# Performance work log

Hardware: AMD Instinct MI355X
Metric: run time of the kernel (lower is better)

Reference implementation:

```python
import jax, jax.numpy as jnp
import numpy as np

LATENT = 8
HIDDEN = 16
DFEAT = 16
N_LAYERS = 10
G = 64          # num graphs
NPG = 1024      # nodes per graph
E = G * NPG * 16  # edges (avg degree 16)


def setup_inputs() -> dict:
    key = jax.random.key(0)
    ks = jax.random.split(key, 20)
    n = G * NPG
    x = jax.random.normal(ks[0], (n, DFEAT), dtype=jnp.float32)
    eps = jax.random.normal(ks[1], (n, LATENT), dtype=jnp.float32)
    # edges constrained to lie within a graph (block-diagonal structure)
    g = jax.random.randint(ks[2], (E,), 0, G)
    ls = jax.random.randint(ks[3], (E,), 0, NPG)
    ld = jax.random.randint(ks[4], (E,), 0, NPG)
    edge_index = jnp.stack([g * NPG + ls, g * NPG + ld]).astype(jnp.int32)
    s = 0.1
    inp = {
        "x": x, "eps": eps, "edge_index": edge_index, "num_graphs": G,
        # GIN layer 0 MLP (lazy in_channels -> hidden -> hidden)
        "W0a": jax.random.normal(ks[5], (DFEAT, HIDDEN), jnp.float32) * s,
        "b0a": jnp.zeros((HIDDEN,), jnp.float32),
        "W0b": jax.random.normal(ks[6], (HIDDEN, HIDDEN), jnp.float32) * s,
        "b0b": jnp.zeros((HIDDEN,), jnp.float32),
        # GIN layers 1..9 MLPs, stacked
        "Wa": jax.random.normal(ks[7], (N_LAYERS - 1, HIDDEN, HIDDEN), jnp.float32) * s,
        "ba": jnp.zeros((N_LAYERS - 1, HIDDEN), jnp.float32),
        "Wb": jax.random.normal(ks[8], (N_LAYERS - 1, HIDDEN, HIDDEN), jnp.float32) * s,
        "bb": jnp.zeros((N_LAYERS - 1, HIDDEN), jnp.float32),
        # mean / std heads
        "Wm": jax.random.normal(ks[9], (HIDDEN, LATENT), jnp.float32) * s,
        "bm": jnp.zeros((LATENT,), jnp.float32),
        "Ws": jax.random.normal(ks[10], (HIDDEN, LATENT), jnp.float32) * s,
        "bs": jnp.zeros((LATENT,), jnp.float32),
    }
    return inp


def _gin_encode(x, edge_index, W0a, b0a, W0b, b0b, Wa, ba, Wb, bb):
    n = x.shape[0]
    src, dst = edge_index[0], edge_index[1]

    def conv(h, wa, bia, wb, bib):
        # GINConv, eps=0: MLP((1+eps)*h + sum_{j in N(i)} h_j)
        agg = h + jax.ops.segment_sum(h[src], dst, num_segments=n)
        return jax.nn.relu(agg @ wa + bia) @ wb + bib

    h = jax.nn.relu(conv(x, W0a, b0a, W0b, b0b))
    for i in range(Wa.shape[0]):
        h = conv(h, Wa[i], ba[i], Wb[i], bb[i])
        if i < Wa.shape[0] - 1:  # act between layers, not after the last conv
            h = jax.nn.relu(h)
    return h


def _vae_forward(x, eps, edge_index, num_graphs,
                 W0a, b0a, W0b, b0b, Wa, ba, Wb, bb, Wm, bm, Ws, bs):
    n = x.shape[0]
    npg = n // num_graphs
    h = _gin_encode(x, edge_index, W0a, b0a, W0b, b0b, Wa, ba, Wb, bb)
    mu = h @ Wm + bm
    std = jax.nn.softplus(h @ Ws + bs)
    z = mu + std * eps                      # rsample from Normal(mu, std)
    z3 = z.reshape(num_graphs, npg, LATENT)  # per-graph split (equal sizes)
    # inner-product decode per graph, sigmoid act
    adj_pred = jax.nn.sigmoid(jnp.einsum("gnd,gmd->gnm", z3, z3))
    # to_dense_adj on the block-diagonal edge list
    src, dst = edge_index[0], edge_index[1]
    g = src // npg
    dense_adj = jnp.zeros((num_graphs, npg, npg), jnp.float32)
    dense_adj = dense_adj.at[g, src % npg, dst % npg].set(1.0)
    # BCELoss(reduction='sum') with torch's log clamp at -100
    logp = jnp.clip(jnp.log(adj_pred), -100.0)
    log1mp = jnp.clip(jnp.log1p(-adj_pred), -100.0)
    nll = -jnp.sum(dense_adj * logp + (1.0 - dense_adj) * log1mp)
    # KL(N(mu,std) || N(0,1)), summed
    kl = jnp.sum(-jnp.log(std) + 0.5 * (std * std + mu * mu) - 0.5)
    return nll, kl, adj_pred, dense_adj


def reference(x, eps, edge_index, num_graphs,
              W0a, b0a, W0b, b0b, Wa, ba, Wb, bb, Wm, bm, Ws, bs):
    return _vae_forward(x, eps, edge_index, num_graphs,
                        W0a, b0a, W0b, b0b, Wa, ba, Wb, bb, Wm, bm, Ws, bs)
```

## Files before the change

kernel.cpp:

```cpp
#include <hip/hip_runtime.h>
#include <cstddef>

#define G 64
#define NPG 1024
#define NNODES 65536
#define NEDGE 1048576
#define BCAP 48
#define LCAP 32
#define HSTR 20
#define ZTR 1028
#define ADJ_ELEMS 67108864ull
#define BM_WORDS 2097152

typedef float f32x4 __attribute__((ext_vector_type(4)));
typedef float f32x2 __attribute__((ext_vector_type(2)));
typedef unsigned u32x4 __attribute__((ext_vector_type(4)));

__global__ __launch_bounds__(1024) void k_init(int* __restrict__ cnt, float* __restrict__ acc,
                                               unsigned* __restrict__ bm) {
  int i = blockIdx.x * 1024 + threadIdx.x;
  cnt[i] = 0;
  if (i < 2) acc[i] = 0.0f;
  u32x4 z = {0u, 0u, 0u, 0u};
  u32x4* b4 = (u32x4*)bm;
  for (int k = i; k < BM_WORDS / 4; k += 65536) b4[k] = z;
}

__global__ __launch_bounds__(256) void k_build(const int* __restrict__ ei,
                                               int* __restrict__ cnt,
                                               unsigned short* __restrict__ colb,
                                               unsigned* __restrict__ bm) {
  int t = blockIdx.x * 256 + threadIdx.x;
  const int4* sp = (const int4*)ei;
  const int4* dp = (const int4*)(ei + NEDGE);
  int4 s4 = sp[t];
  int4 d4 = dp[t];
  int ss[4] = {s4.x, s4.y, s4.z, s4.w};
  int dd[4] = {d4.x, d4.y, d4.z, d4.w};
  #pragma unroll
  for (int q = 0; q < 4; ++q) {
    int src = ss[q], dst = dd[q];
    int p = atomicAdd(&cnt[dst], 1);
    if (p < BCAP) colb[(size_t)dst * BCAP + p] = (unsigned short)(src & (NPG - 1));
    int gg = src >> 10, ls = src & (NPG - 1), ld = dst & (NPG - 1);
    atomicOr(&bm[gg * 32768 + ls * 32 + (ld >> 5)], 1u << (ld & 31));
  }
}

__global__ __launch_bounds__(1024) void k_gin(
    const float* __restrict__ x, const float* __restrict__ eps,
    const int* __restrict__ cnt, const unsigned short* __restrict__ colb,
    const float* __restrict__ W0a, const float* __restrict__ b0a,
    const float* __restrict__ W0b, const float* __restrict__ b0b,
    const float* __restrict__ Wa, const float* __restrict__ ba,
    const float* __restrict__ Wb, const float* __restrict__ bb,
    const float* __restrict__ Wm, const float* __restrict__ bm_,
    const float* __restrict__ Ws, const float* __restrict__ bs,
    const unsigned* __restrict__ ebm,
    float* __restrict__ zbuf, float* __restrict__ acc, float* __restrict__ out) {
  __shared__ float hbuf[NPG * HSTR];
  __shared__ unsigned short colc[NPG * LCAP];
  __shared__ float red[16];

  if (blockIdx.x >= G) {
    f32x4* dz = (f32x4*)(out + 2 + ADJ_ELEMS);
    size_t i = (size_t)(blockIdx.x - G) * 1024 + threadIdx.x;
    size_t stride = (size_t)(gridDim.x - G) * 1024;
    for (; i < ADJ_ELEMS / 4; i += stride) {
      unsigned w = ebm[i >> 3];
      int sh = ((int)i & 7) << 2;
      f32x4 v;
      v.x = ((w >> (sh + 0)) & 1) ? 1.f : 0.f;
      v.y = ((w >> (sh + 1)) & 1) ? 1.f : 0.f;
      v.z = ((w >> (sh + 2)) & 1) ? 1.f : 0.f;
      v.w = ((w >> (sh + 3)) & 1) ? 1.f : 0.f;
      __builtin_nontemporal_store(v, &dz[i]);
    }
    return;
  }

  const int g = blockIdx.x;
  const int tid = threadIdx.x;
  const int dv0 = cnt[g * NPG + tid];
  const int dv = (dv0 < BCAP) ? dv0 : BCAP;
  const int dvl = (dv < LCAP) ? dv : LCAP;
  const unsigned short* cl = colb + (size_t)(g * NPG + tid) * BCAP;

  {
    const uint4* rowp = (const uint4*)(colb + (size_t)(g * NPG + tid) * BCAP);
    #pragma unroll
    for (int q = 0; q < 2; ++q) {
    }
    #pragma unroll
    for (int q = 0; q < 4; ++q) {
      uint4 w4 = rowp[q];
      unsigned ws0 = w4.x, ws1 = w4.y, ws2 = w4.z, ws3 = w4.w;
      colc[(q * 8 + 0) * NPG + tid] = (unsigned short)(ws0 & 0xffff);
      colc[(q * 8 + 1) * NPG + tid] = (unsigned short)(ws0 >> 16);
      colc[(q * 8 + 2) * NPG + tid] = (unsigned short)(ws1 & 0xffff);
      colc[(q * 8 + 3) * NPG + tid] = (unsigned short)(ws1 >> 16);
      colc[(q * 8 + 4) * NPG + tid] = (unsigned short)(ws2 & 0xffff);
      colc[(q * 8 + 5) * NPG + tid] = (unsigned short)(ws2 >> 16);
      colc[(q * 8 + 6) * NPG + tid] = (unsigned short)(ws3 & 0xffff);
      colc[(q * 8 + 7) * NPG + tid] = (unsigned short)(ws3 >> 16);
    }
  }

  {
    const float4* xg = (const float4*)(x + (size_t)g * (NPG * 16));
    for (int idx = tid; idx < NPG * 4; idx += 1024) {
      float4 v = xg[idx];
      *(float4*)(hbuf + (idx >> 2) * HSTR + (idx & 3) * 4) = v;
    }
  }
  __syncthreads();

  for (int l = 0; l < 10; ++l) {
    const float* Aw = (l == 0) ? W0a : Wa + (l - 1) * 256;
    const float* Ab = (l == 0) ? b0a : ba + (l - 1) * 16;
    const float* Bw = (l == 0) ? W0b : Wb + (l - 1) * 256;
    const float* Bb = (l == 0) ? b0b : bb + (l - 1) * 16;

    float4 a0 = *(const float4*)(hbuf + tid * HSTR + 0);
    float4 a1 = *(const float4*)(hbuf + tid * HSTR + 4);
    float4 a2 = *(const float4*)(hbuf + tid * HSTR + 8);
    float4 a3 = *(const float4*)(hbuf + tid * HSTR + 12);
    for (int k = 0; k < dvl; ++k) {
      int ls = colc[k * NPG + tid];
      const float* hp = hbuf + ls * HSTR;
      float4 v0 = *(const float4*)(hp + 0);
      float4 v1 = *(const float4*)(hp + 4);
      float4 v2 = *(const float4*)(hp + 8);
      float4 v3 = *(const float4*)(hp + 12);
      a0.x += v0.x; a0.y += v0.y; a0.z += v0.z; a0.w += v0.w;
      a1.x += v1.x; a1.y += v1.y; a1.z += v1.z; a1.w += v1.w;
      a2.x += v2.x; a2.y += v2.y; a2.z += v2.z; a2.w += v2.w;
      a3.x += v3.x; a3.y += v3.y; a3.z += v3.z; a3.w += v3.w;
    }
    for (int k = LCAP; k < dv; ++k) {
      int ls = cl[k];
      const float* hp = hbuf + ls * HSTR;
      float4 v0 = *(const float4*)(hp + 0);
      float4 v1 = *(const float4*)(hp + 4);
      float4 v2 = *(const float4*)(hp + 8);
      float4 v3 = *(const float4*)(hp + 12);
      a0.x += v0.x; a0.y += v0.y; a0.z += v0.z; a0.w += v0.w;
      a1.x += v1.x; a1.y += v1.y; a1.z += v1.z; a1.w += v1.w;
      a2.x += v2.x; a2.y += v2.y; a2.z += v2.z; a2.w += v2.w;
      a3.x += v3.x; a3.y += v3.y; a3.z += v3.z; a3.w += v3.w;
    }
    float aa[16] = {a0.x, a0.y, a0.z, a0.w, a1.x, a1.y, a1.z, a1.w,
                    a2.x, a2.y, a2.z, a2.w, a3.x, a3.y, a3.z, a3.w};

    float u[16], v[16];
    #pragma unroll
    for (int j = 0; j < 16; ++j) u[j] = Ab[j];
    #pragma unroll
    for (int i = 0; i < 16; ++i) {
      float ai = aa[i];
      #pragma unroll
      for (int j = 0; j < 16; ++j) u[j] += ai * Aw[i * 16 + j];
    }
    #pragma unroll
    for (int j = 0; j < 16; ++j) u[j] = fmaxf(u[j], 0.f);
    #pragma unroll
    for (int j = 0; j < 16; ++j) v[j] = Bb[j];
    #pragma unroll
    for (int i = 0; i < 16; ++i) {
      float ui = u[i];
      #pragma unroll
      for (int j = 0; j < 16; ++j) v[j] += ui * Bw[i * 16 + j];
    }
    const bool rl = (l != 9);
    __syncthreads();
    #pragma unroll
    for (int j4 = 0; j4 < 4; ++j4) {
      float4 w;
      w.x = rl ? fmaxf(v[j4 * 4 + 0], 0.f) : v[j4 * 4 + 0];
      w.y = rl ? fmaxf(v[j4 * 4 + 1], 0.f) : v[j4 * 4 + 1];
      w.z = rl ? fmaxf(v[j4 * 4 + 2], 0.f) : v[j4 * 4 + 2];
      w.w = rl ? fmaxf(v[j4 * 4 + 3], 0.f) : v[j4 * 4 + 3];
      *(float4*)(hbuf + tid * HSTR + j4 * 4) = w;
    }
    __syncthreads();
  }

  float hv[16];
  #pragma unroll
  for (int i = 0; i < 16; ++i) hv[i] = hbuf[tid * HSTR + i];

  float mu[8], st[8];
  #pragma unroll
  for (int m = 0; m < 8; ++m) { mu[m] = bm_[m]; st[m] = bs[m]; }
  #pragma unroll
  for (int i = 0; i < 16; ++i) {
    float hi = hv[i];
    #pragma unroll
    for (int m = 0; m < 8; ++m) { mu[m] += hi * Wm[i * 8 + m]; st[m] += hi * Ws[i * 8 + m]; }
  }
  #pragma unroll
  for (int m = 0; m < 8; ++m) {
    float s = st[m];
    st[m] = fmaxf(s, 0.f) + log1pf(__expf(-fabsf(s)));
  }
  int gid = g * NPG + tid;
  float4 e0 = *(const float4*)(eps + (size_t)gid * 8);
  float4 e1 = *(const float4*)(eps + (size_t)gid * 8 + 4);
  float ev[8] = {e0.x, e0.y, e0.z, e0.w, e1.x, e1.y, e1.z, e1.w};
  float zv[8];
  float klp = 0.f;
  #pragma unroll
  for (int m = 0; m < 8; ++m) {
    zv[m] = mu[m] + st[m] * ev[m];
    klp += -__logf(st[m]) + 0.5f * (st[m] * st[m] + mu[m] * mu[m]) - 0.5f;
  }
  *(float4*)(zbuf + (size_t)gid * 8) = make_float4(zv[0], zv[1], zv[2], zv[3]);
  *(float4*)(zbuf + (size_t)gid * 8 + 4) = make_float4(zv[4], zv[5], zv[6], zv[7]);

  for (int o = 32; o > 0; o >>= 1) klp += __shfl_down(klp, o, 64);
  if ((tid & 63) == 0) red[tid >> 6] = klp;
  __syncthreads();
  if (tid == 0) {
    float s = 0.f;
    for (int i = 0; i < 16; ++i) s += red[i];
    atomicAdd(&acc[1], s);
  }
}

__device__ __forceinline__ float elem_p(float sv, int bit, float& accl) {
  float t = __expf(-sv);
  float p = __builtin_amdgcn_rcpf(1.f + t);
  float lp, lm;
  if (t > 3.0e38f)             { lp = -100.f; lm = 0.f; }
  else if (t < 5.9604645e-08f) { lp = 0.f;    lm = -100.f; }
  else { float q = __logf(1.f + t); lp = -q; lm = -sv - q; }
  accl += bit ? lp : lm;
  return p;
}

__global__ __launch_bounds__(256) void k_adj(const float* __restrict__ zbuf,
                                             const unsigned* __restrict__ ebm,
                                             float* __restrict__ out,
                                             float* __restrict__ acc) {
  __shared__ float zt[8 * ZTR];
  __shared__ float red[4];
  const int tid = threadIdx.x;
  const int g = blockIdx.x >> 6;
  const int i0 = (blockIdx.x & 63) << 4;

  {
    const float4* zg = (const float4*)(zbuf + (size_t)g * (NPG * 8));
    #pragma unroll
    for (int it = 0; it < 8; ++it) {
      int idx = tid + it * 256;
      float4 v = zg[idx];
      int j = idx >> 1, db = (idx & 1) << 2;
      zt[(db + 0) * ZTR + j] = v.x;
      zt[(db + 1) * ZTR + j] = v.y;
      zt[(db + 2) * ZTR + j] = v.z;
      zt[(db + 3) * ZTR + j] = v.w;
    }
  }
  __syncthreads();

  const int w = tid >> 6;
  const int l = tid & 63;
  float accl = 0.f;

  for (int ir = 0; ir < 4; ++ir) {
    const int i = i0 + (w << 2) + ir;
    float zi[8];
    #pragma unroll
    for (int d = 0; d < 8; ++d) zi[d] = zt[d * ZTR + i];
    const unsigned* bmrow = ebm + g * 32768 + i * 32;
    float* orow = out + 2 + (size_t)g * (NPG * NPG) + (size_t)i * NPG;
    #pragma unroll
    for (int jp = 0; jp < 4; ++jp) {
      const int j0 = (l << 2) + (jp << 8);
      float s0 = 0.f, s1 = 0.f, s2 = 0.f, s3 = 0.f;
      #pragma unroll
      for (int d = 0; d < 8; ++d) {
        float4 zr = *(const float4*)(zt + d * ZTR + j0);
        float zd = zi[d];
        s0 += zd * zr.x; s1 += zd * zr.y; s2 += zd * zr.z; s3 += zd * zr.w;
      }
      unsigned bits = (bmrow[j0 >> 5] >> (j0 & 31)) & 15u;
      float p0 = elem_p(s0, bits & 1, accl);
      float p1 = elem_p(s1, (bits >> 1) & 1, accl);
      float p2 = elem_p(s2, (bits >> 2) & 1, accl);
      float p3 = elem_p(s3, (bits >> 3) & 1, accl);
      f32x2 v0 = {p0, p1}, v1 = {p2, p3};
      f32x2* dp = (f32x2*)(orow + j0);
      __builtin_nontemporal_store(v0, &dp[0]);
      __builtin_nontemporal_store(v1, &dp[1]);
    }
  }

  for (int o = 32; o > 0; o >>= 1) accl += __shfl_down(accl, o, 64);
  if (l == 0) red[w] = accl;
  __syncthreads();
  if (tid == 0) atomicAdd(&acc[0], red[0] + red[1] + red[2] + red[3]);
}

__global__ void k_fin(const float* __restrict__ acc, float* __restrict__ out) {
  if (threadIdx.x == 0 && blockIdx.x == 0) {
    out[0] = -acc[0];
    out[1] = acc[1];
  }
}

extern "C" void kernel_launch(void* const* d_in, const int* in_sizes, int n_in,
                              void* d_out, int out_size, void* d_ws, size_t ws_size,
                              hipStream_t stream) {
  const float* x   = (const float*)d_in[0];
  const float* eps = (const float*)d_in[1];
  const int*   ei  = (const int*)d_in[2];
  const float* W0a = (const float*)d_in[4];
  const float* b0a = (const float*)d_in[5];
  const float* W0b = (const float*)d_in[6];
  const float* b0b = (const float*)d_in[7];
  const float* Wa  = (const float*)d_in[8];
  const float* ba  = (const float*)d_in[9];
  const float* Wb  = (const float*)d_in[10];
  const float* bb  = (const float*)d_in[11];
  const float* Wm  = (const float*)d_in[12];
  const float* bm  = (const float*)d_in[13];
  const float* Ws  = (const float*)d_in[14];
  const float* bs  = (const float*)d_in[15];
  float* out = (float*)d_out;

  int* cnt             = (int*)d_ws;
  unsigned short* colb = (unsigned short*)(cnt + NNODES);
  float* zbuf          = (float*)(colb + (size_t)NNODES * BCAP);
  unsigned* ebm        = (unsigned*)(zbuf + (size_t)NNODES * 8);
  float* acc           = (float*)(ebm + BM_WORDS);

  k_init<<<64, 1024, 0, stream>>>(cnt, acc, ebm);
  k_build<<<1024, 256, 0, stream>>>(ei, cnt, colb, ebm);
  k_gin<<<256, 1024, 0, stream>>>(x, eps, cnt, colb,
                                  W0a, b0a, W0b, b0b, Wa, ba, Wb, bb,
                                  Wm, bm, Ws, bs, ebm, zbuf, acc, out);
  k_adj<<<4096, 256, 0, stream>>>(zbuf, ebm, out, acc);
  k_fin<<<1, 64, 0, stream>>>(acc, out);
}
```

Measured before the change: 330.2 us.

## Replace per-node neighbor lists with transposed adjacency bitmap plus duplicate list

The edge build now stores only a destination-major adjacency bitmap, drops the per-node atomic counters and column buffer, and records duplicate edges in a small per-graph list. The GIN kernel derives each node's neighbor list by scanning its bitmap row, with overflow handling in shared memory. The dense-adjacency writer and the adjacency/loss kernel read the transposed bitmap through shared memory. This removes the atomicAdd-based CSR fill and the per-node list traffic, at the cost of bitmap scanning in the GIN kernel and transposed bit lookups in the later kernels.

```diff
diff --git a/kernel.cpp b/kernel.cpp
--- a/kernel.cpp
+++ b/kernel.cpp
@@ -5,31 +5,32 @@
 #define NPG 1024
 #define NNODES 65536
 #define NEDGE 1048576
-#define BCAP 48
-#define LCAP 32
+#define CCAP 36
 #define HSTR 20
 #define ZTR 1028
 #define ADJ_ELEMS 67108864ull
 #define BM_WORDS 2097152
+#define DCAP 1024
 
 typedef float f32x4 __attribute__((ext_vector_type(4)));
 typedef float f32x2 __attribute__((ext_vector_type(2)));
 typedef unsigned u32x4 __attribute__((ext_vector_type(4)));
 
-__global__ __launch_bounds__(1024) void k_init(int* __restrict__ cnt, float* __restrict__ acc,
-                                               unsigned* __restrict__ bm) {
+__global__ __launch_bounds__(1024) void k_init(unsigned* __restrict__ bm2,
+                                               int* __restrict__ dupcnt,
+                                               float* __restrict__ acc) {
   int i = blockIdx.x * 1024 + threadIdx.x;
-  cnt[i] = 0;
+  if (i < G) dupcnt[i] = 0;
   if (i < 2) acc[i] = 0.0f;
   u32x4 z = {0u, 0u, 0u, 0u};
-  u32x4* b4 = (u32x4*)bm;
+  u32x4* b4 = (u32x4*)bm2;
   for (int k = i; k < BM_WORDS / 4; k += 65536) b4[k] = z;
 }
 
 __global__ __launch_bounds__(256) void k_build(const int* __restrict__ ei,
-                                               int* __restrict__ cnt,
-                                               unsigned short* __restrict__ colb,
-                                               unsigned* __restrict__ bm) {
+                                               unsigned* __restrict__ bm2,
+                                               unsigned* __restrict__ dupl,
+                                               int* __restrict__ dupcnt) {
   int t = blockIdx.x * 256 + threadIdx.x;
   const int4* sp = (const int4*)ei;
   const int4* dp = (const int4*)(ei + NEDGE);
@@ -40,71 +41,67 @@
   #pragma unroll
   for (int q = 0; q < 4; ++q) {
     int src = ss[q], dst = dd[q];
-    int p = atomicAdd(&cnt[dst], 1);
-    if (p < BCAP) colb[(size_t)dst * BCAP + p] = (unsigned short)(src & (NPG - 1));
     int gg = src >> 10, ls = src & (NPG - 1), ld = dst & (NPG - 1);
-    atomicOr(&bm[gg * 32768 + ls * 32 + (ld >> 5)], 1u << (ld & 31));
+    unsigned bit = 1u << (ls & 31);
+    unsigned old = atomicOr(&bm2[(size_t)(gg * NPG + ld) * 32 + (ls >> 5)], bit);
+    if (old & bit) {
+      int p = atomicAdd(&dupcnt[gg], 1);
+      if (p < DCAP) dupl[gg * DCAP + p] = ((unsigned)ld << 16) | (unsigned)ls;
+    }
   }
 }
 
 __global__ __launch_bounds__(1024) void k_gin(
     const float* __restrict__ x, const float* __restrict__ eps,
-    const int* __restrict__ cnt, const unsigned short* __restrict__ colb,
+    const unsigned* __restrict__ bm2, const unsigned* __restrict__ dupl,
+    const int* __restrict__ dupcnt,
     const float* __restrict__ W0a, const float* __restrict__ b0a,
     const float* __restrict__ W0b, const float* __restrict__ b0b,
     const float* __restrict__ Wa, const float* __restrict__ ba,
     const float* __restrict__ Wb, const float* __restrict__ bb,
     const float* __restrict__ Wm, const float* __restrict__ bm_,
     const float* __restrict__ Ws, const float* __restrict__ bs,
-    const unsigned* __restrict__ ebm,
     float* __restrict__ zbuf, float* __restrict__ acc, float* __restrict__ out) {
   __shared__ float hbuf[NPG * HSTR];
-  __shared__ unsigned short colc[NPG * LCAP];
+  __shared__ unsigned short colc[NPG * CCAP];
+  __shared__ unsigned dupl_s[DCAP];
+  __shared__ int ovl_s[64];
+  __shared__ int ovn;
   __shared__ float red[16];
 
   if (blockIdx.x >= G) {
-    f32x4* dz = (f32x4*)(out + 2 + ADJ_ELEMS);
-    size_t i = (size_t)(blockIdx.x - G) * 1024 + threadIdx.x;
-    size_t stride = (size_t)(gridDim.x - G) * 1024;
-    for (; i < ADJ_ELEMS / 4; i += stride) {
-      unsigned w = ebm[i >> 3];
-      int sh = ((int)i & 7) << 2;
-      f32x4 v;
-      v.x = ((w >> (sh + 0)) & 1) ? 1.f : 0.f;
-      v.y = ((w >> (sh + 1)) & 1) ? 1.f : 0.f;
-      v.z = ((w >> (sh + 2)) & 1) ? 1.f : 0.f;
-      v.w = ((w >> (sh + 3)) & 1) ? 1.f : 0.f;
-      __builtin_nontemporal_store(v, &dz[i]);
+    unsigned* tw = (unsigned*)hbuf;
+    const int tid = threadIdx.x;
+    for (int c = (int)blockIdx.x - G; c < G * 32; c += (int)gridDim.x - G) {
+      int g = c >> 5, w = c & 31;
+      tw[tid] = bm2[(size_t)(g * NPG + tid) * 32 + w];
+      __syncthreads();
+      float* ob = out + 2 + (size_t)g * (NPG * NPG) + (size_t)(w * 32) * NPG;
+      #pragma unroll
+      for (int it = 0; it < 8; ++it) {
+        int idx = tid + it * 1024;
+        int lsl = idx >> 8;
+        int ld0 = (idx & 255) << 2;
+        u32x4 wb = *(const u32x4*)(tw + ld0);
+        f32x4 v;
+        v.x = ((wb.x >> lsl) & 1) ? 1.f : 0.f;
+        v.y = ((wb.y >> lsl) & 1) ? 1.f : 0.f;
+        v.z = ((wb.z >> lsl) & 1) ? 1.f : 0.f;
+        v.w = ((wb.w >> lsl) & 1) ? 1.f : 0.f;
+        __builtin_nontemporal_store(v, (f32x4*)(ob + (size_t)lsl * NPG + ld0));
+      }
+      __syncthreads();
     }
     return;
   }
 
   const int g = blockIdx.x;
   const int tid = threadIdx.x;
-  const int dv0 = cnt[g * NPG + tid];
-  const int dv = (dv0 < BCAP) ? dv0 : BCAP;
-  const int dvl = (dv < LCAP) ? dv : LCAP;
-  const unsigned short* cl = colb + (size_t)(g * NPG + tid) * BCAP;
-
-  {
-    const uint4* rowp = (const uint4*)(colb + (size_t)(g * NPG + tid) * BCAP);
-    #pragma unroll
-    for (int q = 0; q < 2; ++q) {
-    }
-    #pragma unroll
-    for (int q = 0; q < 4; ++q) {
-      uint4 w4 = rowp[q];
-      unsigned ws0 = w4.x, ws1 = w4.y, ws2 = w4.z, ws3 = w4.w;
-      colc[(q * 8 + 0) * NPG + tid] = (unsigned short)(ws0 & 0xffff);
-      colc[(q * 8 + 1) * NPG + tid] = (unsigned short)(ws0 >> 16);
-      colc[(q * 8 + 2) * NPG + tid] = (unsigned short)(ws1 & 0xffff);
-      colc[(q * 8 + 3) * NPG + tid] = (unsigned short)(ws1 >> 16);
-      colc[(q * 8 + 4) * NPG + tid] = (unsigned short)(ws2 & 0xffff);
-      colc[(q * 8 + 5) * NPG + tid] = (unsigned short)(ws2 >> 16);
-      colc[(q * 8 + 6) * NPG + tid] = (unsigned short)(ws3 & 0xffff);
-      colc[(q * 8 + 7) * NPG + tid] = (unsigned short)(ws3 >> 16);
-    }
-  }
+
+  int D = dupcnt[g];
+  if (D > DCAP) D = DCAP;
+  if (tid == 0) ovn = 0;
+  for (int e = tid; e < D; e += 1024) dupl_s[e] = dupl[g * DCAP + e];
 
   {
     const float4* xg = (const float4*)(x + (size_t)g * (NPG * 16));
@@ -114,6 +111,40 @@
     }
   }
   __syncthreads();
+
+  int dv = 0;
+  {
+    const unsigned* myrow = bm2 + (size_t)(g * NPG + tid) * 32;
+    #pragma unroll
+    for (int w = 0; w < 8; ++w) {
+      u32x4 w4 = *(const u32x4*)(myrow + w * 4);
+      unsigned ws4[4] = {w4.x, w4.y, w4.z, w4.w};
+      #pragma unroll
+      for (int q = 0; q < 4; ++q) {
+        unsigned m = ws4[q];
+        int base = (w * 4 + q) * 32;
+        while (m) {
+          int b = __builtin_ctz(m); m &= m - 1;
+          int ls = base + b;
+          if (dv < CCAP) colc[dv * NPG + tid] = (unsigned short)ls;
+          else { int p = atomicAdd(&ovn, 1); if (p < 64) ovl_s[p] = (tid << 16) | ls; }
+          ++dv;
+        }
+      }
+    }
+    for (int e = 0; e < D; ++e) {
+      unsigned ent = dupl_s[e];
+      if ((int)(ent >> 16) == tid) {
+        int ls = (int)(ent & (NPG - 1));
+        if (dv < CCAP) colc[dv * NPG + tid] = (unsigned short)ls;
+        else { int p = atomicAdd(&ovn, 1); if (p < 64) ovl_s[p] = (tid << 16) | ls; }
+        ++dv;
+      }
+    }
+  }
+  const int dvl = (dv < CCAP) ? dv : CCAP;
+  __syncthreads();
+  const int OV = (ovn < 64) ? ovn : 64;
 
   for (int l = 0; l < 10; ++l) {
     const float* Aw = (l == 0) ? W0a : Wa + (l - 1) * 256;
@@ -137,17 +168,19 @@
       a2.x += v2.x; a2.y += v2.y; a2.z += v2.z; a2.w += v2.w;
       a3.x += v3.x; a3.y += v3.y; a3.z += v3.z; a3.w += v3.w;
     }
-    for (int k = LCAP; k < dv; ++k) {
-      int ls = cl[k];
-      const float* hp = hbuf + ls * HSTR;
-      float4 v0 = *(const float4*)(hp + 0);
-      float4 v1 = *(const float4*)(hp + 4);
-      float4 v2 = *(const float4*)(hp + 8);
-      float4 v3 = *(const float4*)(hp + 12);
-      a0.x += v0.x; a0.y += v0.y; a0.z += v0.z; a0.w += v0.w;
-      a1.x += v1.x; a1.y += v1.y; a1.z += v1.z; a1.w += v1.w;
-      a2.x += v2.x; a2.y += v2.y; a2.z += v2.z; a2.w += v2.w;
-      a3.x += v3.x; a3.y += v3.y; a3.z += v3.z; a3.w += v3.w;
+    for (int e = 0; e < OV; ++e) {
+      int ent = ovl_s[e];
+      if ((ent >> 16) == tid) {
+        const float* hp = hbuf + (ent & (NPG - 1)) * HSTR;
+        float4 v0 = *(const float4*)(hp + 0);
+        float4 v1 = *(const float4*)(hp + 4);
+        float4 v2 = *(const float4*)(hp + 8);
+        float4 v3 = *(const float4*)(hp + 12);
+        a0.x += v0.x; a0.y += v0.y; a0.z += v0.z; a0.w += v0.w;
+        a1.x += v1.x; a1.y += v1.y; a1.z += v1.z; a1.w += v1.w;
+        a2.x += v2.x; a2.y += v2.y; a2.z += v2.z; a2.w += v2.w;
+        a3.x += v3.x; a3.y += v3.y; a3.z += v3.z; a3.w += v3.w;
+      }
     }
     float aa[16] = {a0.x, a0.y, a0.z, a0.w, a1.x, a1.y, a1.z, a1.w,
                     a2.x, a2.y, a2.z, a2.w, a3.x, a3.y, a3.z, a3.w};
@@ -239,10 +272,11 @@
 }
 
 __global__ __launch_bounds__(256) void k_adj(const float* __restrict__ zbuf,
-                                             const unsigned* __restrict__ ebm,
+                                             const unsigned* __restrict__ bm2,
                                              float* __restrict__ out,
                                              float* __restrict__ acc) {
   __shared__ float zt[8 * ZTR];
+  __shared__ unsigned tw[NPG];
   __shared__ float red[4];
   const int tid = threadIdx.x;
   const int g = blockIdx.x >> 6;
@@ -260,6 +294,9 @@
       zt[(db + 2) * ZTR + j] = v.z;
       zt[(db + 3) * ZTR + j] = v.w;
     }
+    const int wq = i0 >> 5;
+    for (int idx = tid; idx < NPG; idx += 256)
+      tw[idx] = bm2[(size_t)(g * NPG + idx) * 32 + wq];
   }
   __syncthreads();
 
@@ -269,10 +306,10 @@
 
   for (int ir = 0; ir < 4; ++ir) {
     const int i = i0 + (w << 2) + ir;
+    const int sh = i & 31;
     float zi[8];
     #pragma unroll
     for (int d = 0; d < 8; ++d) zi[d] = zt[d * ZTR + i];
-    const unsigned* bmrow = ebm + g * 32768 + i * 32;
     float* orow = out + 2 + (size_t)g * (NPG * NPG) + (size_t)i * NPG;
     #pragma unroll
     for (int jp = 0; jp < 4; ++jp) {
@@ -284,11 +321,11 @@
         float zd = zi[d];
         s0 += zd * zr.x; s1 += zd * zr.y; s2 += zd * zr.z; s3 += zd * zr.w;
       }
-      unsigned bits = (bmrow[j0 >> 5] >> (j0 & 31)) & 15u;
-      float p0 = elem_p(s0, bits & 1, accl);
-      float p1 = elem_p(s1, (bits >> 1) & 1, accl);
-      float p2 = elem_p(s2, (bits >> 2) & 1, accl);
-      float p3 = elem_p(s3, (bits >> 3) & 1, accl);
+      u32x4 wb = *(const u32x4*)(tw + j0);
+      float p0 = elem_p(s0, (wb.x >> sh) & 1, accl);
+      float p1 = elem_p(s1, (wb.y >> sh) & 1, accl);
+      float p2 = elem_p(s2, (wb.z >> sh) & 1, accl);
+      float p3 = elem_p(s3, (wb.w >> sh) & 1, accl);
       f32x2 v0 = {p0, p1}, v1 = {p2, p3};
       f32x2* dp = (f32x2*)(orow + j0);
       __builtin_nontemporal_store(v0, &dp[0]);
@@ -329,17 +366,17 @@
   const float* bs  = (const float*)d_in[15];
   float* out = (float*)d_out;
 
-  int* cnt             = (int*)d_ws;
-  unsigned short* colb = (unsigned short*)(cnt + NNODES);
-  float* zbuf          = (float*)(colb + (size_t)NNODES * BCAP);
-  unsigned* ebm        = (unsigned*)(zbuf + (size_t)NNODES * 8);
-  float* acc           = (float*)(ebm + BM_WORDS);
-
-  k_init<<<64, 1024, 0, stream>>>(cnt, acc, ebm);
-  k_build<<<1024, 256, 0, stream>>>(ei, cnt, colb, ebm);
-  k_gin<<<256, 1024, 0, stream>>>(x, eps, cnt, colb,
+  unsigned* bm2  = (unsigned*)d_ws;
+  unsigned* dupl = bm2 + BM_WORDS;
+  int* dupcnt    = (int*)(dupl + G * DCAP);
+  float* zbuf    = (float*)(dupcnt + G);
+  float* acc     = zbuf + (size_t)NNODES * 8;
+
+  k_init<<<64, 1024, 0, stream>>>(bm2, dupcnt, acc);
+  k_build<<<1024, 256, 0, stream>>>(ei, bm2, dupl, dupcnt);
+  k_gin<<<256, 1024, 0, stream>>>(x, eps, bm2, dupl, dupcnt,
                                   W0a, b0a, W0b, b0b, Wa, ba, Wb, bb,
-                                  Wm, bm, Ws, bs, ebm, zbuf, acc, out);
-  k_adj<<<4096, 256, 0, stream>>>(zbuf, ebm, out, acc);
+                                  Wm, bm, Ws, bs, zbuf, acc, out);
+  k_adj<<<4096, 256, 0, stream>>>(zbuf, bm2, out, acc);
   k_fin<<<1, 64, 0, stream>>>(acc, out);
 }
```

New measurement: 355.8 us. 1.08x slower.
